# Kernel optimization log

Measured on AMD Instinct MI355X. Metric: run time of the kernel, lower is better.

## Reference

```python
import jax, jax.numpy as jnp
import numpy as np


def setup_inputs() -> dict:
    B, N, D, M = 512, 128, 768, 32  # bags, num_class, embed_dim, max bag size
    rng = np.random.default_rng(0)
    sizes = rng.integers(8, 25, size=B)  # variable bag sizes in [8, 24], all <= M
    offsets = np.concatenate([[0], np.cumsum(sizes)]).astype(np.int32)
    nsum = int(offsets[-1])
    scope = np.stack([offsets[:-1], offsets[1:]], axis=1)  # (B, 2) [start, end)

    key = jax.random.key(0)
    k1, k2, k3 = jax.random.split(key, 3)
    rep = jax.random.normal(k1, (nsum, D), dtype=jnp.float32)
    fc_weight = jax.random.normal(k2, (N, D), dtype=jnp.float32) * 0.02
    fc_bias = jax.random.normal(k3, (N,), dtype=jnp.float32) * 0.02
    return {
        "rep": rep,
        "fc_weight": fc_weight,
        "fc_bias": fc_bias,
        "scope": jnp.asarray(scope),
        "max_bag": M,
    }


def reference(rep, fc_weight, fc_bias, scope, max_bag):
    """IntraBagAttention forward (train=False, bag_size=0 branch), ragged bags
    rewritten as padded/masked dense ops.

    rep:       (nsum, D) sentence-encoder outputs
    fc_weight: (N, D), fc_bias: (N,)
    scope:     (B, 2) int [start, end) per bag; max_bag: static int pad bound
    returns:   (B, N) per-relation bag scores
    """
    nsum = rep.shape[0]
    starts = scope[:, 0]
    sizes = scope[:, 1] - scope[:, 0]
    pos = jnp.arange(max_bag)
    idx = jnp.clip(starts[:, None] + pos[None, :], 0, nsum - 1)  # (B, M)
    valid = pos[None, :] < sizes[:, None]                        # (B, M)
    bag = rep[idx]                                               # (B, M, D)

    # att_score = rep @ fc.weight.data.T ; .data => no grad through this use
    w_att = jax.lax.stop_gradient(fc_weight)
    att = jnp.einsum('bmd,nd->bnm', bag, w_att)                  # (B, N, M)
    att = jnp.where(valid[:, None, :], att, -jnp.inf)
    sm = jax.nn.softmax(att, axis=-1)                            # per-bag softmax over sentences

    # weighted segment sum: one attended rep per relation per bag
    rfer = jnp.einsum('bnm,bmd->bnd', sm, bag)                   # (B, N, D)

    # fc(rep_for_each_rel) -> (B, N, N); softmax over classes; take diagonal
    full = jnp.einsum('bnd,kd->bnk', rfer, fc_weight) + fc_bias  # (B, N, N)
    probs = jax.nn.softmax(full, axis=-1)
    return jnp.diagonal(probs, axis1=1, axis2=2)                 # (B, N)
```

## Files before the change

kernel.cpp:

```cpp
#include <hip/hip_runtime.h>
#include <math.h>

#define B_BAGS 512
#define N_REL  128
#define D_DIM  768

typedef __attribute__((ext_vector_type(8))) short  bf16x8;
typedef __attribute__((ext_vector_type(4))) float  f32x4;

__device__ inline unsigned pack_hi(float f0, float f1) {
    return __builtin_amdgcn_perm(__float_as_uint(f1), __float_as_uint(f0), 0x07060302u);
}
__device__ inline float trunc_res(float f) {
    return f - __uint_as_float(__float_as_uint(f) & 0xFFFF0000u);
}

__global__ void build_bfrag(const float* __restrict__ W, unsigned* __restrict__ Bfrag) {
    int flat = blockIdx.x * 256 + threadIdx.x;
    int lane = flat & 63;
    int tile = (flat >> 6) & 7;
    int s    = flat >> 9;
    int n  = tile * 16 + (lane & 15);
    int k0 = s * 32 + (lane >> 4) * 8;
    const float* src = &W[n * D_DIM + k0];
    float f[8];
    #pragma unroll
    for (int j = 0; j < 8; ++j) f[j] = src[j];
    unsigned hi[4], lo[4];
    #pragma unroll
    for (int q = 0; q < 4; ++q) {
        hi[q] = pack_hi(f[2*q], f[2*q+1]);
        lo[q] = pack_hi(trunc_res(f[2*q]), trunc_res(f[2*q+1]));
    }
    unsigned base = (unsigned)(((s * 8 + tile) * 2) * 64 + lane) * 4;
    *(uint4*)&Bfrag[base]          = make_uint4(hi[0], hi[1], hi[2], hi[3]);
    *(uint4*)&Bfrag[base + 64 * 4] = make_uint4(lo[0], lo[1], lo[2], lo[3]);
}

__global__ __launch_bounds__(512, 2) void h_gemm(
    const float*    __restrict__ rep,
    const unsigned* __restrict__ Bfrag,
    float*          __restrict__ H,
    int nsum)
{
    __shared__ unsigned As[2][32][68];

    const int t     = threadIdx.x;
    const int strip = blockIdx.x;

    const int wv   = t >> 6;
    const int lane = t & 63;
    const int nl15 = lane & 15;
    const int lg   = lane >> 4;
    const int mt   = wv & 1;
    const int nh   = wv >> 1;

    const int srow = t >> 4;
    const int scq  = t & 15;
    int grow = strip * 32 + srow;
    grow = (grow > nsum - 1) ? (nsum - 1) : grow;
    const float* srp = &rep[(size_t)grow * D_DIM + scq * 8];

    f32x4 acc[2][2];
    #pragma unroll
    for (int ntl = 0; ntl < 2; ++ntl) {
        acc[ntl][0] = f32x4{0.f, 0.f, 0.f, 0.f};
        acc[ntl][1] = f32x4{0.f, 0.f, 0.f, 0.f};
    }

    const int arow = mt * 16 + nl15;

    #pragma unroll
    for (int st = 0; st < 6; ++st) {
        if (st) __syncthreads();
        {
            const float4 v0 = *(const float4*)&srp[st * 128];
            const float4 v1 = *(const float4*)&srp[st * 128 + 4];
            const float f[8] = {v0.x, v0.y, v0.z, v0.w, v1.x, v1.y, v1.z, v1.w};
            unsigned hi[4], lo[4];
            #pragma unroll
            for (int w = 0; w < 4; ++w) {
                hi[w] = pack_hi(f[2*w], f[2*w+1]);
                lo[w] = pack_hi(trunc_res(f[2*w]), trunc_res(f[2*w+1]));
            }
            *(uint4*)&As[0][srow][scq * 4] = make_uint4(hi[0], hi[1], hi[2], hi[3]);
            *(uint4*)&As[1][srow][scq * 4] = make_uint4(lo[0], lo[1], lo[2], lo[3]);
        }
        __syncthreads();

        #pragma unroll
        for (int g = 0; g < 4; ++g) {
            const int gs = st * 4 + g;
            const bf16x8 ah = *(const bf16x8*)&As[0][arow][g * 16 + lg * 4];
            const bf16x8 al = *(const bf16x8*)&As[1][arow][g * 16 + lg * 4];
            #pragma unroll
            for (int ntl = 0; ntl < 2; ++ntl) {
                const int nt = nh * 2 + ntl;
                const bf16x8 bh = *(const bf16x8*)&Bfrag[((gs * 8 + nt) * 2 + 0) * 256 + lane * 4];
                const bf16x8 bl = *(const bf16x8*)&Bfrag[((gs * 8 + nt) * 2 + 1) * 256 + lane * 4];
                acc[ntl][0] = __builtin_amdgcn_mfma_f32_16x16x32_bf16(ah, bh, acc[ntl][0], 0, 0, 0);
                acc[ntl][1] = __builtin_amdgcn_mfma_f32_16x16x32_bf16(ah, bl, acc[ntl][1], 0, 0, 0);
                acc[ntl][1] = __builtin_amdgcn_mfma_f32_16x16x32_bf16(al, bh, acc[ntl][1], 0, 0, 0);
            }
        }
    }

    const int rowb = strip * 32 + mt * 16 + lg * 4;
    #pragma unroll
    for (int ntl = 0; ntl < 2; ++ntl) {
        const int col = (nh * 2 + ntl) * 16 + nl15;
        #pragma unroll
        for (int r = 0; r < 4; ++r)
            H[(size_t)(rowb + r) * N_REL + col] = acc[ntl][0][r] + acc[ntl][1][r];
    }
}

__global__ __launch_bounds__(512, 2) void bag_out(
    const float* __restrict__ H,
    const float* __restrict__ bias,
    const int*   __restrict__ scope,
    float*       __restrict__ out,
    int nsum)
{
    __shared__ unsigned Gfrag[8 * 2 * 64 * 4];
    __shared__ unsigned SMfrag[8 * 2 * 64 * 4];

    const int t = threadIdx.x;
    const int b = blockIdx.x;
    const int start = scope[2 * b];
    const int size  = scope[2 * b + 1] - start;

    const int wv   = t >> 6;
    const int lane = t & 63;
    const int nl15 = lane & 15;
    const int lg   = lane >> 4;
    const int T    = wv;

    float gv[2][4], smv[2][4];
    #pragma unroll
    for (int mt = 0; mt < 2; ++mt)
        #pragma unroll
        for (int r = 0; r < 4; ++r) {
            int row = start + mt * 16 + lg * 4 + r;
            row = (row > nsum - 1) ? (nsum - 1) : row;
            gv[mt][r] = H[(size_t)row * N_REL + T * 16 + nl15];
        }

    float vmax = -INFINITY;
    #pragma unroll
    for (int mt = 0; mt < 2; ++mt)
        #pragma unroll
        for (int r = 0; r < 4; ++r) {
            const int m = mt * 16 + lg * 4 + r;
            if (m < size) vmax = fmaxf(vmax, gv[mt][r]);
        }
    vmax = fmaxf(vmax, __shfl_xor(vmax, 16));
    vmax = fmaxf(vmax, __shfl_xor(vmax, 32));

    float ssum = 0.f;
    #pragma unroll
    for (int mt = 0; mt < 2; ++mt)
        #pragma unroll
        for (int r = 0; r < 4; ++r) {
            const int m = mt * 16 + lg * 4 + r;
            float e = (m < size) ? __expf(gv[mt][r] - vmax) : 0.f;
            smv[mt][r] = e;
            ssum += e;
        }
    ssum += __shfl_xor(ssum, 16);
    ssum += __shfl_xor(ssum, 32);
    const float inv = 1.f / ssum;
    #pragma unroll
    for (int mt = 0; mt < 2; ++mt)
        #pragma unroll
        for (int r = 0; r < 4; ++r) smv[mt][r] *= inv;

    #pragma unroll
    for (int mt = 0; mt < 2; ++mt)
        #pragma unroll
        for (int rp = 0; rp < 4; rp += 2) {
            const int m     = mt * 16 + lg * 4 + rp;
            const int lane2 = (m >> 3) * 16 + nl15;
            const int word  = (m >> 1) & 3;
            const int ihi = ((T * 2 + 0) * 64 + lane2) * 4 + word;
            const int ilo = ((T * 2 + 1) * 64 + lane2) * 4 + word;
            Gfrag[ihi]  = pack_hi(gv[mt][rp], gv[mt][rp + 1]);
            Gfrag[ilo]  = pack_hi(trunc_res(gv[mt][rp]), trunc_res(gv[mt][rp + 1]));
            SMfrag[ihi] = pack_hi(smv[mt][rp], smv[mt][rp + 1]);
            SMfrag[ilo] = pack_hi(trunc_res(smv[mt][rp]), trunc_res(smv[mt][rp + 1]));
        }
    __syncthreads();

    float bias_r[8];
    #pragma unroll
    for (int ct = 0; ct < 8; ++ct) bias_r[ct] = bias[ct * 16 + nl15];

    f32x4 facc[8];
    #pragma unroll
    for (int ct = 0; ct < 8; ++ct) facc[ct] = f32x4{0.f, 0.f, 0.f, 0.f};

    const bf16x8 ah2 = *(const bf16x8*)&SMfrag[((T * 2 + 0) * 64 + lane) * 4];
    const bf16x8 al2 = *(const bf16x8*)&SMfrag[((T * 2 + 1) * 64 + lane) * 4];
    #pragma unroll
    for (int ct = 0; ct < 8; ++ct) {
        const bf16x8 bh = *(const bf16x8*)&Gfrag[((ct * 2 + 0) * 64 + lane) * 4];
        const bf16x8 bl = *(const bf16x8*)&Gfrag[((ct * 2 + 1) * 64 + lane) * 4];
        facc[ct] = __builtin_amdgcn_mfma_f32_16x16x32_bf16(ah2, bh, facc[ct], 0, 0, 0);
        facc[ct] = __builtin_amdgcn_mfma_f32_16x16x32_bf16(ah2, bl, facc[ct], 0, 0, 0);
        facc[ct] = __builtin_amdgcn_mfma_f32_16x16x32_bf16(al2, bh, facc[ct], 0, 0, 0);
    }

    #pragma unroll
    for (int r = 0; r < 4; ++r) {
        float s[8];
        #pragma unroll
        for (int ct = 0; ct < 8; ++ct) s[ct] = facc[ct][r] + bias_r[ct];

        float mx = s[0];
        #pragma unroll
        for (int ct = 1; ct < 8; ++ct) mx = fmaxf(mx, s[ct]);
        mx = fmaxf(mx, __shfl_xor(mx, 1));
        mx = fmaxf(mx, __shfl_xor(mx, 2));
        mx = fmaxf(mx, __shfl_xor(mx, 4));
        mx = fmaxf(mx, __shfl_xor(mx, 8));

        float l = 0.f;
        #pragma unroll
        for (int ct = 0; ct < 8; ++ct) l += __expf(s[ct] - mx);
        l += __shfl_xor(l, 1);
        l += __shfl_xor(l, 2);
        l += __shfl_xor(l, 4);
        l += __shfl_xor(l, 8);

        const int nl = lg * 4 + r;
        float sd = s[0];
        #pragma unroll
        for (int ct = 1; ct < 8; ++ct) sd = (ct == T) ? s[ct] : sd;
        if (nl15 == nl) {
            out[b * N_REL + T * 16 + nl] = __expf(sd - mx) / l;
        }
    }
}

extern "C" void kernel_launch(void* const* d_in, const int* in_sizes, int n_in,
                              void* d_out, int out_size, void* d_ws, size_t ws_size,
                              hipStream_t stream) {
    const float* rep   = (const float*)d_in[0];
    const float* W     = (const float*)d_in[1];
    const float* bias  = (const float*)d_in[2];
    const int*   scope = (const int*)d_in[3];

    const int nsum   = in_sizes[0] / D_DIM;
    const int strips = (nsum + 31) >> 5;

    unsigned* Bfrag = (unsigned*)d_ws;
    float*    H     = (float*)((char*)d_ws + 393216);

    build_bfrag<<<48, 256, 0, stream>>>(W, Bfrag);
    h_gemm<<<strips, 512, 0, stream>>>(rep, Bfrag, H, nsum);
    bag_out<<<B_BAGS, 512, 0, stream>>>(H, bias, scope, (float*)d_out, nsum);
}
```

Baseline: 97.53 us.

## Split H GEMM into 16-row strips and two K-halves with partial sums

Changes h_gemm from 32-row strips over the full K dimension with 512 threads to 16-row strips with 256 threads and a second grid dimension that splits K=768 into two halves. Each half writes its own partial H buffer, and bag_out adds the two partials when it loads H. The goal is more blocks and better CU occupancy on a small GEMM (~8k rows). In exchange it doubles H writes and reads and needs more workspace, and each block no longer shares B fragment loads across M tiles.

```diff
diff --git a/kernel.cpp b/kernel.cpp
--- a/kernel.cpp
+++ b/kernel.cpp
@@ -37,29 +37,28 @@
     *(uint4*)&Bfrag[base + 64 * 4] = make_uint4(lo[0], lo[1], lo[2], lo[3]);
 }
 
-__global__ __launch_bounds__(512, 2) void h_gemm(
+__global__ __launch_bounds__(256, 8) void h_gemm(
     const float*    __restrict__ rep,
     const unsigned* __restrict__ Bfrag,
-    float*          __restrict__ H,
-    int nsum)
+    float*          __restrict__ Hp,
+    int nsum, int hstride)
 {
-    __shared__ unsigned As[2][32][68];
+    __shared__ unsigned As[2][16][68];
 
     const int t     = threadIdx.x;
     const int strip = blockIdx.x;
+    const int chunk = blockIdx.y;
 
     const int wv   = t >> 6;
     const int lane = t & 63;
     const int nl15 = lane & 15;
     const int lg   = lane >> 4;
-    const int mt   = wv & 1;
-    const int nh   = wv >> 1;
 
     const int srow = t >> 4;
     const int scq  = t & 15;
-    int grow = strip * 32 + srow;
+    int grow = strip * 16 + srow;
     grow = (grow > nsum - 1) ? (nsum - 1) : grow;
-    const float* srp = &rep[(size_t)grow * D_DIM + scq * 8];
+    const float* srp = &rep[(size_t)grow * D_DIM + chunk * 384 + scq * 8];
 
     f32x4 acc[2][2];
     #pragma unroll
@@ -68,10 +67,8 @@
         acc[ntl][1] = f32x4{0.f, 0.f, 0.f, 0.f};
     }
 
-    const int arow = mt * 16 + nl15;
-
-    #pragma unroll
-    for (int st = 0; st < 6; ++st) {
+    #pragma unroll
+    for (int st = 0; st < 3; ++st) {
         if (st) __syncthreads();
         {
             const float4 v0 = *(const float4*)&srp[st * 128];
@@ -90,12 +87,12 @@
 
         #pragma unroll
         for (int g = 0; g < 4; ++g) {
-            const int gs = st * 4 + g;
-            const bf16x8 ah = *(const bf16x8*)&As[0][arow][g * 16 + lg * 4];
-            const bf16x8 al = *(const bf16x8*)&As[1][arow][g * 16 + lg * 4];
+            const int gs = chunk * 12 + st * 4 + g;
+            const bf16x8 ah = *(const bf16x8*)&As[0][nl15][g * 16 + lg * 4];
+            const bf16x8 al = *(const bf16x8*)&As[1][nl15][g * 16 + lg * 4];
             #pragma unroll
             for (int ntl = 0; ntl < 2; ++ntl) {
-                const int nt = nh * 2 + ntl;
+                const int nt = wv * 2 + ntl;
                 const bf16x8 bh = *(const bf16x8*)&Bfrag[((gs * 8 + nt) * 2 + 0) * 256 + lane * 4];
                 const bf16x8 bl = *(const bf16x8*)&Bfrag[((gs * 8 + nt) * 2 + 1) * 256 + lane * 4];
                 acc[ntl][0] = __builtin_amdgcn_mfma_f32_16x16x32_bf16(ah, bh, acc[ntl][0], 0, 0, 0);
@@ -105,10 +102,11 @@
         }
     }
 
-    const int rowb = strip * 32 + mt * 16 + lg * 4;
+    float* H = Hp + (size_t)chunk * hstride;
+    const int rowb = strip * 16 + lg * 4;
     #pragma unroll
     for (int ntl = 0; ntl < 2; ++ntl) {
-        const int col = (nh * 2 + ntl) * 16 + nl15;
+        const int col = (wv * 2 + ntl) * 16 + nl15;
         #pragma unroll
         for (int r = 0; r < 4; ++r)
             H[(size_t)(rowb + r) * N_REL + col] = acc[ntl][0][r] + acc[ntl][1][r];
@@ -116,7 +114,7 @@
 }
 
 __global__ __launch_bounds__(512, 2) void bag_out(
-    const float* __restrict__ H,
+    const float* __restrict__ Hp, int hstride,
     const float* __restrict__ bias,
     const int*   __restrict__ scope,
     float*       __restrict__ out,
@@ -143,7 +141,8 @@
         for (int r = 0; r < 4; ++r) {
             int row = start + mt * 16 + lg * 4 + r;
             row = (row > nsum - 1) ? (nsum - 1) : row;
-            gv[mt][r] = H[(size_t)row * N_REL + T * 16 + nl15];
+            const float* p = &Hp[(size_t)row * N_REL + T * 16 + nl15];
+            gv[mt][r] = p[0] + p[(size_t)hstride];
         }
 
     float vmax = -INFINITY;
@@ -250,13 +249,15 @@
     const float* bias  = (const float*)d_in[2];
     const int*   scope = (const int*)d_in[3];
 
-    const int nsum   = in_sizes[0] / D_DIM;
-    const int strips = (nsum + 31) >> 5;
+    const int nsum    = in_sizes[0] / D_DIM;
+    const int strips  = (nsum + 15) >> 4;
+    const int hstride = strips * 16 * N_REL;
 
     unsigned* Bfrag = (unsigned*)d_ws;
-    float*    H     = (float*)((char*)d_ws + 393216);
+    float*    Hp    = (float*)((char*)d_ws + 393216);
 
     build_bfrag<<<48, 256, 0, stream>>>(W, Bfrag);
-    h_gemm<<<strips, 512, 0, stream>>>(rep, Bfrag, H, nsum);
-    bag_out<<<B_BAGS, 512, 0, stream>>>(H, bias, scope, (float*)d_out, nsum);
-}
+    h_gemm<<<dim3(strips, 2), 256, 0, stream>>>(rep, Bfrag, Hp, nsum, hstride);
+    bag_out<<<B_BAGS, 512, 0, stream>>>(Hp, hstride, bias, scope,
+                                        (float*)d_out, nsum);
+}
```

Measured after the change: 93.25 us. -4.4%, faster.
